# Kernel optimization log

Measured on AMD Instinct MI355X. Metric: run time of the kernel, lower is better.

## Reference

```python
import jax, jax.numpy as jnp
import numpy as np

# ---- system_parameters stand-ins (external module not in source) ----
D1, D2, D3 = 0.1, 1.0, 2.0
SIZE_X, SIZE_D = 5.0, 5.0
POWER_CONVERT = 10.0  # max power for opt_QoS stand-in
B, H, C = 8192, 96, 4
K1, K2 = 256, 256
D_IN = C + 2


def gamma_calculation(Hn):
    idx = np.arange(Hn)
    J = idx[:, None]  # row j
    I = idx[None, :]  # col i (time t)
    off = (D1 / 8.0 * (SIZE_X + SIZE_D) + D2 / 4.0) * (0.25 ** np.clip(I - 1 - J, 0, None))
    q = np.where(I == J, 2.0 * D1 * SIZE_X + D2, np.where(I > J, off, 0.0))
    gamma_list = q.sum(1)
    # Gamma_mat[j, t] = sum_{i>=t} q[j, i] for t >= j, else 0
    gmat = np.cumsum(q[:, ::-1], axis=1)[:, ::-1]
    gmat = np.where(I >= J, gmat, 0.0)
    return gamma_list.astype(np.float32), gmat.astype(np.float32), q.astype(np.float32)


def opt_qos(state, demand, power_max):
    # stand-in for external opt_QoS: action that serves demand and drains state
    # (nominal efficiency 0.8), capped at max power
    return jnp.minimum(jax.nn.relu(state + demand) / 0.8, power_max)


def setup_inputs() -> dict:
    key = jax.random.key(0)
    ks = jax.random.split(key, 9)
    kaiming = lambda k, shape: jax.random.normal(k, shape, jnp.float32) * np.sqrt(2.0 / shape[1])
    return {
        "policy_in_c": jax.random.uniform(ks[0], (B, H, C), jnp.float32) * 5.0,
        "trans_noise": jax.random.uniform(ks[1], (B, H, 1), jnp.float32) * 0.1,
        "demand_noise": jax.random.uniform(ks[2], (B, H, 1), jnp.float32) * 0.1,
        "action_pre": jax.random.uniform(ks[3], (B, 1), jnp.float32),
        "state_pre": jax.random.uniform(ks[4], (B, 1), jnp.float32) * 5.0,
        "Lambda": jnp.array([0.1], jnp.float32),
        "Budget": jnp.array([10.0], jnp.float32),
        "W1": kaiming(ks[5], (K1, D_IN)),
        "b1": jnp.zeros((K1,), jnp.float32),
        "W2": kaiming(ks[6], (K2, K1)),
        "b2": jnp.zeros((K2,), jnp.float32),
        "W3": kaiming(ks[7], (1, K2)),
        "b3": jnp.zeros((1,), jnp.float32),
    }


def reference(policy_in_c, trans_noise, demand_noise, action_pre, state_pre,
              Lambda, Budget, W1, b1, W2, b2, W3, b3):
    Bsz, Hn = policy_in_c.shape[0], policy_in_c.shape[1]
    gl_np, gmat_np, q_np = gamma_calculation(Hn)
    gamma_list = jnp.asarray(gl_np)                       # [H]
    q_cols = jnp.asarray(q_np.T)                          # q_cols[t] = q_mat[:, t]
    g_cols = jnp.asarray(np.concatenate([gmat_np[:, 1:].T,
                                         np.zeros((1, Hn), np.float32)], 0))  # g_cols[t] = Gamma_mat[:, t+1]
    per_step = Lambda * D3 + Budget / Hn                  # [1]
    bgt0 = per_step * jnp.ones((Bsz, 1), jnp.float32)

    def mlp(x):
        h1 = jax.nn.relu(x @ W1.T + b1)
        h2 = jax.nn.relu(h1 @ W2.T + b2)
        return jax.nn.relu(h2 @ W3.T + b3)

    def step(carry, xs):
        action_, state_, bgt, cum_c, dev, ad_prev = carry
        t, feat, noise, noise2, Gamma, q_col, g_col = xs
        a_ml = mlp(jnp.concatenate([feat, action_, state_], -1))
        demand = feat[:, :1]
        a_prior = opt_qos(state_, demand, POWER_CONVERT)
        sign = (a_ml < a_prior).astype(a_ml.dtype) * 2.0 - 1.0
        a_out = a_ml + jax.nn.relu(jnp.abs(a_ml - a_prior) - bgt / Gamma) * sign
        new_state = jnp.minimum(
            jax.nn.relu(state_ * (1.0 - noise2) + demand - (0.8 + noise) * a_out), 15.0)
        # ---- non-final-step branch (dev zero-padded to [B,H] so full matvec == sliced matmul) ----
        c_cost = D1 * new_state ** 2 + D2 * new_state + D3
        ad_new = jnp.abs(a_out - a_prior)
        dev_new = dev.at[:, t].set(ad_new[:, 0])
        cum_d = dev_new @ q_col                            # [B]
        c_prior = jnp.maximum(D3, c_cost - cum_d[:, None])
        cum_c_new = cum_c + (1.0 + Lambda) * c_prior - c_cost
        cum_d_g = dev_new @ g_col                          # [B]
        bgt_if = jnp.maximum(
            jax.nn.relu(bgt + per_step - ad_new * Gamma),
            cum_c_new - cum_d_g[:, None] + Lambda * D3 + (Budget / Hn) * (t + 2.0))
        # final step uses the stale action_diff from the previous iteration (as in source)
        bgt_else = jax.nn.relu(bgt + per_step - ad_prev * Gamma)
        is_last = t == Hn - 1
        bgt_next = jnp.where(is_last, bgt_else, bgt_if)
        cum_c_next = jnp.where(is_last, cum_c, cum_c_new)
        return (a_out, new_state, bgt_next, cum_c_next, dev_new, ad_new), a_out

    xs = (jnp.arange(Hn),
          jnp.transpose(policy_in_c, (1, 0, 2)),
          jnp.transpose(trans_noise, (1, 0, 2)),
          jnp.transpose(demand_noise, (1, 0, 2)),
          gamma_list, q_cols, g_cols)
    carry0 = (action_pre, state_pre, bgt0, jnp.zeros((Bsz, 1), jnp.float32),
              jnp.zeros((Bsz, Hn), jnp.float32), jnp.zeros((Bsz, 1), jnp.float32))
    _, ys = jax.lax.scan(step, carry0, xs)                 # ys: [H, B, 1]
    return jnp.transpose(ys[:, :, 0])                      # [B, H]
```

## Files before the change

### kernel.cpp

```cpp
#include <hip/hip_runtime.h>
#include <stdint.h>
#include <stddef.h>

typedef float    f32x4 __attribute__((ext_vector_type(4)));
typedef float    f32x2 __attribute__((ext_vector_type(2)));
typedef _Float16 f16x4 __attribute__((ext_vector_type(4)));
typedef _Float16 f16x8 __attribute__((ext_vector_type(8)));

#define HH 96
#define MROWS 16
#define OCT 136
#define NSTR 32
#define OSTR 100

#define DPP_ADD(v, ctrl) \
    ((v) + __builtin_bit_cast(float, __builtin_amdgcn_update_dpp( \
        0, __builtin_bit_cast(int, (v)), (ctrl), 0xF, 0xF, true)))

__launch_bounds__(256, 2)
__global__ void policy_scan_kernel(
    const float* __restrict__ policy,
    const float* __restrict__ noiseT,
    const float* __restrict__ noiseD,
    const float* __restrict__ action_pre,
    const float* __restrict__ state_pre,
    const float* __restrict__ Lambda1,
    const float* __restrict__ Budget1,
    const float* __restrict__ W1,
    const float* __restrict__ b1,
    const float* __restrict__ W2,
    const float* __restrict__ b2,
    const float* __restrict__ W3,
    const float* __restrict__ b3,
    float* __restrict__ out)
{
    __shared__ __attribute__((aligned(16))) float    featLDS[HH*MROWS*4];
    __shared__ __attribute__((aligned(16))) float    noiseTD[HH*NSTR];
    __shared__ __attribute__((aligned(16))) _Float16 h1LDS[32*OCT];
    __shared__ __attribute__((aligned(16))) float    partialLDS[MROWS*4];
    __shared__ __attribute__((aligned(16))) float    tblLDS[HH*4];
    __shared__ __attribute__((aligned(16))) float    outLDS[MROWS*OSTR];

    const int tid  = threadIdx.x;
    const int wave = tid >> 6;
    const int lane = tid & 63;
    const int l16  = lane & 15;
    const int lq   = lane >> 4;
    const int r0   = blockIdx.x * MROWS;

    {
        const f32x4* src = (const f32x4*)(policy + (size_t)r0 * HH * 4);
        #pragma unroll
        for (int i = 0; i < 6; ++i) {
            int idx = i*256 + tid;
            int row = idx / 96, t = idx - row*96;
            *(f32x4*)&featLDS[(t*MROWS + row)*4] = src[idx];
        }
        const float* s1 = noiseT + (size_t)r0 * HH;
        const float* s2 = noiseD + (size_t)r0 * HH;
        #pragma unroll
        for (int i = 0; i < 6; ++i) {
            int idx = i*256 + tid;
            int row = idx / 96, t = idx - row*96;
            noiseTD[t*NSTR + row*2    ] = s1[idx];
            noiseTD[t*NSTR + row*2 + 1] = s2[idx];
        }
    }
    const float lam  = Lambda1[0];
    const float budH = Budget1[0] * (1.0f/96.0f);
    const float b3s  = b3[0];
    const float per_step = lam * 2.0f + budH;
    if (tid < HH) {
        float e  = __builtin_exp2f(-2.0f * (float)(95 - tid));
        float ft = 0.5f * (1.0f - e);
        float G  = 2.0f + ft;
        *(f32x4*)&tblLDS[tid*4] = f32x4{ft, G, 1.0f/G, lam*2.0f + budH*((float)tid + 2.0f)};
    }

    f16x8 bfr[4][8];
    float b2v[4], w3v[4];
    #pragma unroll
    for (int tt = 0; tt < 4; ++tt) {
        const int n = wave*64 + tt*16 + l16;
        const float* wrow = W2 + (size_t)n * 256;
        #pragma unroll
        for (int kc = 0; kc < 8; ++kc) {
            const int k0 = kc*32 + lq*8;
            f32x4 u0 = *(const f32x4*)(wrow + k0);
            f32x4 u1 = *(const f32x4*)(wrow + k0 + 4);
            f16x8 v;
            v[0]=(_Float16)u0[0]; v[1]=(_Float16)u0[1]; v[2]=(_Float16)u0[2]; v[3]=(_Float16)u0[3];
            v[4]=(_Float16)u1[0]; v[5]=(_Float16)u1[1]; v[6]=(_Float16)u1[2]; v[7]=(_Float16)u1[3];
            bfr[tt][kc] = v;
        }
        b2v[tt] = b2[n];
        w3v[tt] = W3[n];
    }

    f16x8 w1A[4];
    #pragma unroll
    for (int tt = 0; tt < 4; ++tt) {
        f16x8 w = {};
        if (lq == 0) {
            const int nn = wave*64 + tt*16 + l16;
            #pragma unroll
            for (int j = 0; j < 6; ++j) w[j] = (_Float16)W1[nn*6 + j];
            w[6] = (_Float16)b1[nn];
        }
        w1A[tt] = w;
    }

    const int h1wbase = (wave*8 + (lq>>1))*OCT + l16*8 + (lq&1)*4;
    const int h1r     = lq*OCT + l16*8;

    float stA = action_pre[r0 + l16];
    float stS = state_pre[r0 + l16];
    float stB = per_step, stC = 0.0f, stSS = 0.0f, stAD = 0.0f;
    __syncthreads();

    #pragma unroll 1
    for (int t = 0; t < HH; ++t) {
        f32x4 f = *(const f32x4*)&featLDS[(t*MROWS + l16)*4];
        float dem = f[0];
        f16x8 xB = {};
        if (lq == 0) {
            xB[0]=(_Float16)f[0]; xB[1]=(_Float16)f[1];
            xB[2]=(_Float16)f[2]; xB[3]=(_Float16)f[3];
            xB[4]=(_Float16)stA;  xB[5]=(_Float16)stS;
            xB[6]=(_Float16)1.0f;
        }
        #pragma unroll
        for (int tt = 0; tt < 4; ++tt) {
            f32x4 g = {0.f,0.f,0.f,0.f};
            g = __builtin_amdgcn_mfma_f32_16x16x32_f16(w1A[tt], xB, g, 0, 0, 0);
            f16x4 hv;
            #pragma unroll
            for (int r = 0; r < 4; ++r) hv[r] = (_Float16)fmaxf(g[r], 0.0f);
            *(f16x4*)&h1LDS[h1wbase + tt*(2*OCT)] = hv;
        }
        __syncthreads();

        f32x4 acc[4];
        #pragma unroll
        for (int tt = 0; tt < 4; ++tt) acc[tt] = f32x4{0.f,0.f,0.f,0.f};
        #pragma unroll
        for (int kc = 0; kc < 8; ++kc) {
            f16x8 a = *(const f16x8*)&h1LDS[h1r + kc*(4*OCT)];
            #pragma unroll
            for (int tt = 0; tt < 4; ++tt)
                acc[tt] = __builtin_amdgcn_mfma_f32_16x16x32_f16(a, bfr[tt][kc], acc[tt], 0, 0, 0);
        }

        #pragma unroll
        for (int r = 0; r < 4; ++r) {
            float v = 0.f;
            #pragma unroll
            for (int tt = 0; tt < 4; ++tt)
                v = fmaf(w3v[tt], fmaxf(acc[tt][r] + b2v[tt], 0.0f), v);
            v = DPP_ADD(v, 0xB1);
            v = DPP_ADD(v, 0x4E);
            v = DPP_ADD(v, 0x124);
            v = DPP_ADD(v, 0x128);
            if (l16 == 0) partialLDS[(lq*4 + r)*4 + wave] = v;
        }
        __syncthreads();

        f32x4 q  = *(const f32x4*)&partialLDS[l16*4];
        f32x4 tb = *(const f32x4*)&tblLDS[t*4];
        f32x2 nz = *(const f32x2*)&noiseTD[t*NSTR + l16*2];
        float psum = (q[0] + q[1]) + (q[2] + q[3]);
        float a_ml   = fmaxf(psum + b3s, 0.0f);
        float a_prior = fminf(fmaxf(stS + dem, 0.0f) * 1.25f, 10.0f);
        float sgn    = (a_ml < a_prior) ? 1.0f : -1.0f;
        float a_out  = fmaf(fmaxf(fabsf(a_ml - a_prior) - stB * tb[2], 0.0f), sgn, a_ml);
        float ns     = fminf(fmaxf(stS * (1.0f - nz[1]) + dem - (0.8f + nz[0]) * a_out, 0.0f), 15.0f);
        float c_cost = fmaf(fmaf(0.1f, ns, 1.0f), ns, 2.0f);
        float ad_new = fabsf(a_out - a_prior);
        float cum_dv = fmaf(2.0f, ad_new, 0.375f * stSS);
        float c_prior = fmaxf(2.0f, c_cost - cum_dv);
        float cum_c_new = stC + (1.0f + lam) * c_prior - c_cost;
        float T      = fmaf(0.25f, stSS, ad_new);
        float cum_dg = tb[0] * T;
        float bgt_if = fmaxf(fmaxf(stB + per_step - ad_new * tb[1], 0.0f),
                             cum_c_new - cum_dg + tb[3]);
        float bgt_else = fmaxf(stB + per_step - stAD * tb[1], 0.0f);
        if (t == HH - 1) { stB = bgt_else; }
        else             { stB = bgt_if; stC = cum_c_new; }
        stSS = T;
        stAD = ad_new;
        stA  = a_out;
        stS  = ns;
        if (tid < MROWS) outLDS[tid*OSTR + t] = a_out;
    }

    __syncthreads();
    float* oslice = out + (size_t)r0 * HH;
    #pragma unroll
    for (int i = 0; i < 3; ++i) {
        int idx = (i*256 + tid) * 2;
        int row = idx / 96, c = idx - row*96;
        f32x2 v = { outLDS[row*OSTR + c], outLDS[row*OSTR + c + 1] };
        *(f32x2*)&oslice[idx] = v;
    }
}

extern "C" void kernel_launch(void* const* d_in, const int* in_sizes, int n_in,
                              void* d_out, int out_size, void* d_ws, size_t ws_size,
                              hipStream_t stream) {
    policy_scan_kernel<<<dim3(8192 / MROWS), dim3(256), 0, stream>>>(
        (const float*)d_in[0],
        (const float*)d_in[1],
        (const float*)d_in[2],
        (const float*)d_in[3],
        (const float*)d_in[4],
        (const float*)d_in[5],
        (const float*)d_in[6],
        (const float*)d_in[7],
        (const float*)d_in[8],
        (const float*)d_in[9],
        (const float*)d_in[10],
        (const float*)d_in[11],
        (const float*)d_in[12],
        (float*)d_out);
}
```

Measured before the change: 222.8 us.

## Compute layer-1 redundantly per wave in registers, dropping the h1 LDS round-trip and barrier

Each wave now computes every layer-1 activation itself with 16x16x16 MFMAs and feeds the packed f16 result straight into the layer-2 MFMA A operand. This removes the h1 shared-memory buffer and one __syncthreads per timestep from the serial scan loop. The partial-sum buffer is double-buffered so a single barrier per step is enough. The cost is 4x redundant layer-1 MFMA work and more registers for the W1 fragments, and W2's k-index mapping is reordered to match the new register layout.

```diff
diff --git a/kernel.cpp b/kernel.cpp
--- a/kernel.cpp
+++ b/kernel.cpp
@@ -4,18 +4,20 @@
 
 typedef float    f32x4 __attribute__((ext_vector_type(4)));
 typedef float    f32x2 __attribute__((ext_vector_type(2)));
+typedef _Float16 f16x2 __attribute__((ext_vector_type(2)));
 typedef _Float16 f16x4 __attribute__((ext_vector_type(4)));
 typedef _Float16 f16x8 __attribute__((ext_vector_type(8)));
 
 #define HH 96
 #define MROWS 16
-#define OCT 136
 #define NSTR 32
 #define OSTR 100
 
 #define DPP_ADD(v, ctrl) \
     ((v) + __builtin_bit_cast(float, __builtin_amdgcn_update_dpp( \
         0, __builtin_bit_cast(int, (v)), (ctrl), 0xF, 0xF, true)))
+
+#define CVT_PK(a, b) __builtin_bit_cast(f16x2, __builtin_amdgcn_cvt_pkrtz((a), (b)))
 
 __launch_bounds__(256, 2)
 __global__ void policy_scan_kernel(
@@ -34,12 +36,11 @@
     const float* __restrict__ b3,
     float* __restrict__ out)
 {
-    __shared__ __attribute__((aligned(16))) float    featLDS[HH*MROWS*4];
-    __shared__ __attribute__((aligned(16))) float    noiseTD[HH*NSTR];
-    __shared__ __attribute__((aligned(16))) _Float16 h1LDS[32*OCT];
-    __shared__ __attribute__((aligned(16))) float    partialLDS[MROWS*4];
-    __shared__ __attribute__((aligned(16))) float    tblLDS[HH*4];
-    __shared__ __attribute__((aligned(16))) float    outLDS[MROWS*OSTR];
+    __shared__ __attribute__((aligned(16))) float featLDS[HH*MROWS*4];
+    __shared__ __attribute__((aligned(16))) float noiseTD[HH*NSTR];
+    __shared__ __attribute__((aligned(16))) float partialLDS[2][MROWS*4];
+    __shared__ __attribute__((aligned(16))) float tblLDS[HH*4];
+    __shared__ __attribute__((aligned(16))) float outLDS[MROWS*OSTR];
 
     const int tid  = threadIdx.x;
     const int wave = tid >> 6;
@@ -85,9 +86,8 @@
         const float* wrow = W2 + (size_t)n * 256;
         #pragma unroll
         for (int kc = 0; kc < 8; ++kc) {
-            const int k0 = kc*32 + lq*8;
-            f32x4 u0 = *(const f32x4*)(wrow + k0);
-            f32x4 u1 = *(const f32x4*)(wrow + k0 + 4);
+            f32x4 u0 = *(const f32x4*)(wrow + kc*32 + lq*4);
+            f32x4 u1 = *(const f32x4*)(wrow + kc*32 + 16 + lq*4);
             f16x8 v;
             v[0]=(_Float16)u0[0]; v[1]=(_Float16)u0[1]; v[2]=(_Float16)u0[2]; v[3]=(_Float16)u0[3];
             v[4]=(_Float16)u1[0]; v[5]=(_Float16)u1[1]; v[6]=(_Float16)u1[2]; v[7]=(_Float16)u1[3];
@@ -97,21 +97,20 @@
         w3v[tt] = W3[n];
     }
 
-    f16x8 w1A[4];
+    f16x4 w1A[16];
     #pragma unroll
-    for (int tt = 0; tt < 4; ++tt) {
-        f16x8 w = {};
+    for (int q2 = 0; q2 < 16; ++q2) {
+        f16x4 w = {};
+        const int nn = q2*16 + l16;
         if (lq == 0) {
-            const int nn = wave*64 + tt*16 + l16;
-            #pragma unroll
-            for (int j = 0; j < 6; ++j) w[j] = (_Float16)W1[nn*6 + j];
-            w[6] = (_Float16)b1[nn];
-        }
-        w1A[tt] = w;
-    }
-
-    const int h1wbase = (wave*8 + (lq>>1))*OCT + l16*8 + (lq&1)*4;
-    const int h1r     = lq*OCT + l16*8;
+            w[0]=(_Float16)W1[nn*6+0]; w[1]=(_Float16)W1[nn*6+1];
+            w[2]=(_Float16)W1[nn*6+2]; w[3]=(_Float16)W1[nn*6+3];
+        } else if (lq == 1) {
+            w[0]=(_Float16)W1[nn*6+4]; w[1]=(_Float16)W1[nn*6+5];
+            w[2]=(_Float16)b1[nn];
+        }
+        w1A[q2] = w;
+    }
 
     float stA = action_pre[r0 + l16];
     float stS = state_pre[r0 + l16];
@@ -120,54 +119,55 @@
 
     #pragma unroll 1
     for (int t = 0; t < HH; ++t) {
-        f32x4 f = *(const f32x4*)&featLDS[(t*MROWS + l16)*4];
-        float dem = f[0];
-        f16x8 xB = {};
+        const f32x4 f  = *(const f32x4*)&featLDS[(t*MROWS + l16)*4];
+        const f32x4 tb = *(const f32x4*)&tblLDS[t*4];
+        const f32x2 nz = *(const f32x2*)&noiseTD[t*NSTR + l16*2];
+        const float dem = f[0];
+
+        f16x4 xB = {};
         if (lq == 0) {
             xB[0]=(_Float16)f[0]; xB[1]=(_Float16)f[1];
             xB[2]=(_Float16)f[2]; xB[3]=(_Float16)f[3];
-            xB[4]=(_Float16)stA;  xB[5]=(_Float16)stS;
-            xB[6]=(_Float16)1.0f;
-        }
-        #pragma unroll
-        for (int tt = 0; tt < 4; ++tt) {
-            f32x4 g = {0.f,0.f,0.f,0.f};
-            g = __builtin_amdgcn_mfma_f32_16x16x32_f16(w1A[tt], xB, g, 0, 0, 0);
-            f16x4 hv;
-            #pragma unroll
-            for (int r = 0; r < 4; ++r) hv[r] = (_Float16)fmaxf(g[r], 0.0f);
-            *(f16x4*)&h1LDS[h1wbase + tt*(2*OCT)] = hv;
-        }
-        __syncthreads();
+        } else if (lq == 1) {
+            xB[0]=(_Float16)stA; xB[1]=(_Float16)stS; xB[2]=(_Float16)1.0f;
+        }
 
         f32x4 acc[4];
         #pragma unroll
-        for (int tt = 0; tt < 4; ++tt) acc[tt] = f32x4{0.f,0.f,0.f,0.f};
+        for (int tt = 0; tt < 4; ++tt)
+            acc[tt] = f32x4{b2v[tt], b2v[tt], b2v[tt], b2v[tt]};
+
         #pragma unroll
         for (int kc = 0; kc < 8; ++kc) {
-            f16x8 a = *(const f16x8*)&h1LDS[h1r + kc*(4*OCT)];
+            const f32x4 z = {0.f, 0.f, 0.f, 0.f};
+            f32x4 g0 = __builtin_amdgcn_mfma_f32_16x16x16f16(w1A[2*kc    ], xB, z, 0, 0, 0);
+            f32x4 g1 = __builtin_amdgcn_mfma_f32_16x16x16f16(w1A[2*kc + 1], xB, z, 0, 0, 0);
+            f16x2 c0 = CVT_PK(g0[0], g0[1]);
+            f16x2 c1 = CVT_PK(g0[2], g0[3]);
+            f16x2 c2 = CVT_PK(g1[0], g1[1]);
+            f16x2 c3 = CVT_PK(g1[2], g1[3]);
+            f16x8 h = {c0[0],c0[1],c1[0],c1[1],c2[0],c2[1],c3[0],c3[1]};
+            const f16x8 hz = {};
+            h = __builtin_elementwise_max(h, hz);
             #pragma unroll
             for (int tt = 0; tt < 4; ++tt)
-                acc[tt] = __builtin_amdgcn_mfma_f32_16x16x32_f16(a, bfr[tt][kc], acc[tt], 0, 0, 0);
+                acc[tt] = __builtin_amdgcn_mfma_f32_16x16x32_f16(h, bfr[tt][kc], acc[tt], 0, 0, 0);
         }
 
         #pragma unroll
         for (int r = 0; r < 4; ++r) {
-            float v = 0.f;
-            #pragma unroll
-            for (int tt = 0; tt < 4; ++tt)
-                v = fmaf(w3v[tt], fmaxf(acc[tt][r] + b2v[tt], 0.0f), v);
+            float s0 = fmaf(w3v[0], fmaxf(acc[0][r], 0.0f), w3v[1] * fmaxf(acc[1][r], 0.0f));
+            float s1 = fmaf(w3v[2], fmaxf(acc[2][r], 0.0f), w3v[3] * fmaxf(acc[3][r], 0.0f));
+            float v = s0 + s1;
             v = DPP_ADD(v, 0xB1);
             v = DPP_ADD(v, 0x4E);
             v = DPP_ADD(v, 0x124);
             v = DPP_ADD(v, 0x128);
-            if (l16 == 0) partialLDS[(lq*4 + r)*4 + wave] = v;
+            if (l16 == 0) partialLDS[t & 1][(lq*4 + r)*4 + wave] = v;
         }
         __syncthreads();
 
-        f32x4 q  = *(const f32x4*)&partialLDS[l16*4];
-        f32x4 tb = *(const f32x4*)&tblLDS[t*4];
-        f32x2 nz = *(const f32x2*)&noiseTD[t*NSTR + l16*2];
+        const f32x4 q = *(const f32x4*)&partialLDS[t & 1][l16*4];
         float psum = (q[0] + q[1]) + (q[2] + q[3]);
         float a_ml   = fmaxf(psum + b3s, 0.0f);
         float a_prior = fminf(fmaxf(stS + dem, 0.0f) * 1.25f, 10.0f);
```

Result: slower. 243.1 us (+9.1%).

## Interleave two independent row groups per block to overlap scan latency

Applied to the files above, without the earlier changes.

Each block now handles two 16-row groups (P and Q) that are software-pipelined. One group's layer-2 MFMAs and scalar recurrence run while the other group's layer-1 and reduction are in flight, which hides the serial dependency chain of the time scan. The LDS staging of features, noise and outputs is removed. Inputs are prefetched one step ahead straight from global memory, and outputs are written directly to global. The b2 bias is folded into the accumulator initialisation. In exchange the block count halves and launch bounds drop to one block per SIMD, and output writes become strided and uncoalesced.

```diff
diff --git a/kernel.cpp b/kernel.cpp
--- a/kernel.cpp
+++ b/kernel.cpp
@@ -8,16 +8,41 @@
 typedef _Float16 f16x8 __attribute__((ext_vector_type(8)));
 
 #define HH 96
-#define MROWS 16
+#define RPB 32
 #define OCT 136
-#define NSTR 32
-#define OSTR 100
 
 #define DPP_ADD(v, ctrl) \
     ((v) + __builtin_bit_cast(float, __builtin_amdgcn_update_dpp( \
         0, __builtin_bit_cast(int, (v)), (ctrl), 0xF, 0xF, true)))
 
-__launch_bounds__(256, 2)
+struct SState { float A, S, B, C, SS, AD; };
+
+__device__ __forceinline__ float scan_update(
+    SState& st, float psum, float dem, f32x2 nz, f32x4 tb,
+    float b3s, float lam, float per_step, bool last)
+{
+    float a_ml   = fmaxf(psum + b3s, 0.0f);
+    float a_prior = fminf(fmaxf(st.S + dem, 0.0f) * 1.25f, 10.0f);
+    float sgn    = (a_ml < a_prior) ? 1.0f : -1.0f;
+    float a_out  = fmaf(fmaxf(fabsf(a_ml - a_prior) - st.B * tb[2], 0.0f), sgn, a_ml);
+    float ns     = fminf(fmaxf(st.S * (1.0f - nz[1]) + dem - (0.8f + nz[0]) * a_out, 0.0f), 15.0f);
+    float c_cost = fmaf(fmaf(0.1f, ns, 1.0f), ns, 2.0f);
+    float ad_new = fabsf(a_out - a_prior);
+    float cum_dv = fmaf(2.0f, ad_new, 0.375f * st.SS);
+    float c_prior = fmaxf(2.0f, c_cost - cum_dv);
+    float cum_c_new = st.C + (1.0f + lam) * c_prior - c_cost;
+    float T      = fmaf(0.25f, st.SS, ad_new);
+    float cum_dg = tb[0] * T;
+    float bgt_if = fmaxf(fmaxf(st.B + per_step - ad_new * tb[1], 0.0f),
+                         cum_c_new - cum_dg + tb[3]);
+    float bgt_else = fmaxf(st.B + per_step - st.AD * tb[1], 0.0f);
+    if (last) { st.B = bgt_else; }
+    else      { st.B = bgt_if; st.C = cum_c_new; }
+    st.SS = T; st.AD = ad_new; st.A = a_out; st.S = ns;
+    return a_out;
+}
+
+__launch_bounds__(256, 1)
 __global__ void policy_scan_kernel(
     const float* __restrict__ policy,
     const float* __restrict__ noiseT,
@@ -34,38 +59,19 @@
     const float* __restrict__ b3,
     float* __restrict__ out)
 {
-    __shared__ __attribute__((aligned(16))) float    featLDS[HH*MROWS*4];
-    __shared__ __attribute__((aligned(16))) float    noiseTD[HH*NSTR];
-    __shared__ __attribute__((aligned(16))) _Float16 h1LDS[32*OCT];
-    __shared__ __attribute__((aligned(16))) float    partialLDS[MROWS*4];
+    __shared__ __attribute__((aligned(16))) _Float16 h1P[32*OCT];
+    __shared__ __attribute__((aligned(16))) _Float16 h1Q[32*OCT];
+    __shared__ __attribute__((aligned(16))) float    partP[16*4];
+    __shared__ __attribute__((aligned(16))) float    partQ[16*4];
     __shared__ __attribute__((aligned(16))) float    tblLDS[HH*4];
-    __shared__ __attribute__((aligned(16))) float    outLDS[MROWS*OSTR];
 
     const int tid  = threadIdx.x;
     const int wave = tid >> 6;
     const int lane = tid & 63;
     const int l16  = lane & 15;
     const int lq   = lane >> 4;
-    const int r0   = blockIdx.x * MROWS;
-
-    {
-        const f32x4* src = (const f32x4*)(policy + (size_t)r0 * HH * 4);
-        #pragma unroll
-        for (int i = 0; i < 6; ++i) {
-            int idx = i*256 + tid;
-            int row = idx / 96, t = idx - row*96;
-            *(f32x4*)&featLDS[(t*MROWS + row)*4] = src[idx];
-        }
-        const float* s1 = noiseT + (size_t)r0 * HH;
-        const float* s2 = noiseD + (size_t)r0 * HH;
-        #pragma unroll
-        for (int i = 0; i < 6; ++i) {
-            int idx = i*256 + tid;
-            int row = idx / 96, t = idx - row*96;
-            noiseTD[t*NSTR + row*2    ] = s1[idx];
-            noiseTD[t*NSTR + row*2 + 1] = s2[idx];
-        }
-    }
+    const int r0   = blockIdx.x * RPB;
+
     const float lam  = Lambda1[0];
     const float budH = Budget1[0] * (1.0f/96.0f);
     const float b3s  = b3[0];
@@ -113,101 +119,166 @@
     const int h1wbase = (wave*8 + (lq>>1))*OCT + l16*8 + (lq&1)*4;
     const int h1r     = lq*OCT + l16*8;
 
-    float stA = action_pre[r0 + l16];
-    float stS = state_pre[r0 + l16];
-    float stB = per_step, stC = 0.0f, stSS = 0.0f, stAD = 0.0f;
+    const float* pP  = policy + (size_t)(r0 + l16)      * (HH*4);
+    const float* pQ  = policy + (size_t)(r0 + 16 + l16) * (HH*4);
+    const float* tPp = noiseT + (size_t)(r0 + l16)      * HH;
+    const float* tQp = noiseT + (size_t)(r0 + 16 + l16) * HH;
+    const float* dPp = noiseD + (size_t)(r0 + l16)      * HH;
+    const float* dQp = noiseD + (size_t)(r0 + 16 + l16) * HH;
+
+    SState stP = { action_pre[r0 + l16],      state_pre[r0 + l16],      per_step, 0.f, 0.f, 0.f };
+    SState stQ = { action_pre[r0 + 16 + l16], state_pre[r0 + 16 + l16], per_step, 0.f, 0.f, 0.f };
+
+    f32x4 fP  = *(const f32x4*)(pP);
+    f32x4 fQ  = *(const f32x4*)(pQ);
+    f32x2 nzP = { tPp[0], dPp[0] };
+    f32x2 nzQ = { tQp[0], dQp[0] };
+
+    f32x4 accP[4], accQ[4];
+    #pragma unroll
+    for (int tt = 0; tt < 4; ++tt) accQ[tt] = f32x4{0.f,0.f,0.f,0.f};
+
+    float demQprev = 0.f;
+    f32x2 nzQprev  = {0.f, 0.f};
+    f32x4 tbQprev  = {0.f, 0.f, 0.f, 0.f};
+
     __syncthreads();
 
     #pragma unroll 1
     for (int t = 0; t < HH; ++t) {
-        f32x4 f = *(const f32x4*)&featLDS[(t*MROWS + l16)*4];
-        float dem = f[0];
-        f16x8 xB = {};
-        if (lq == 0) {
-            xB[0]=(_Float16)f[0]; xB[1]=(_Float16)f[1];
-            xB[2]=(_Float16)f[2]; xB[3]=(_Float16)f[3];
-            xB[4]=(_Float16)stA;  xB[5]=(_Float16)stS;
-            xB[6]=(_Float16)1.0f;
-        }
-        #pragma unroll
-        for (int tt = 0; tt < 4; ++tt) {
-            f32x4 g = {0.f,0.f,0.f,0.f};
-            g = __builtin_amdgcn_mfma_f32_16x16x32_f16(w1A[tt], xB, g, 0, 0, 0);
-            f16x4 hv;
-            #pragma unroll
-            for (int r = 0; r < 4; ++r) hv[r] = (_Float16)fmaxf(g[r], 0.0f);
-            *(f16x4*)&h1LDS[h1wbase + tt*(2*OCT)] = hv;
+        const f32x4 tbP = *(const f32x4*)&tblLDS[t*4];
+
+        {
+            f16x8 xB = {};
+            if (lq == 0) {
+                xB[0]=(_Float16)fP[0]; xB[1]=(_Float16)fP[1];
+                xB[2]=(_Float16)fP[2]; xB[3]=(_Float16)fP[3];
+                xB[4]=(_Float16)stP.A; xB[5]=(_Float16)stP.S;
+                xB[6]=(_Float16)1.0f;
+            }
+            #pragma unroll
+            for (int tt = 0; tt < 4; ++tt) {
+                f32x4 g = {0.f,0.f,0.f,0.f};
+                g = __builtin_amdgcn_mfma_f32_16x16x32_f16(w1A[tt], xB, g, 0, 0, 0);
+                f16x4 hv;
+                #pragma unroll
+                for (int r = 0; r < 4; ++r) hv[r] = (_Float16)fmaxf(g[r], 0.0f);
+                *(f16x4*)&h1P[h1wbase + tt*(2*OCT)] = hv;
+            }
+        }
+
+        if (t > 0) {
+            #pragma unroll
+            for (int r = 0; r < 4; ++r) {
+                float s0 = fmaf(w3v[0], fmaxf(accQ[0][r], 0.0f), w3v[1] * fmaxf(accQ[1][r], 0.0f));
+                float s1 = fmaf(w3v[2], fmaxf(accQ[2][r], 0.0f), w3v[3] * fmaxf(accQ[3][r], 0.0f));
+                float v = s0 + s1;
+                v = DPP_ADD(v, 0xB1); v = DPP_ADD(v, 0x4E);
+                v = DPP_ADD(v, 0x124); v = DPP_ADD(v, 0x128);
+                if (l16 == 0) partQ[(lq*4 + r)*4 + wave] = v;
+            }
         }
         __syncthreads();
 
-        f32x4 acc[4];
-        #pragma unroll
-        for (int tt = 0; tt < 4; ++tt) acc[tt] = f32x4{0.f,0.f,0.f,0.f};
+        #pragma unroll
+        for (int tt = 0; tt < 4; ++tt) accP[tt] = f32x4{b2v[tt], b2v[tt], b2v[tt], b2v[tt]};
         #pragma unroll
         for (int kc = 0; kc < 8; ++kc) {
-            f16x8 a = *(const f16x8*)&h1LDS[h1r + kc*(4*OCT)];
+            f16x8 a = *(const f16x8*)&h1P[h1r + kc*(4*OCT)];
             #pragma unroll
             for (int tt = 0; tt < 4; ++tt)
-                acc[tt] = __builtin_amdgcn_mfma_f32_16x16x32_f16(a, bfr[tt][kc], acc[tt], 0, 0, 0);
+                accP[tt] = __builtin_amdgcn_mfma_f32_16x16x32_f16(a, bfr[tt][kc], accP[tt], 0, 0, 0);
+        }
+
+        const int tn = (t < HH-1) ? t+1 : HH-1;
+        f32x4 fPn  = *(const f32x4*)(pP + tn*4);
+        f32x4 fQn  = *(const f32x4*)(pQ + tn*4);
+        f32x2 nzPn = { tPp[tn], dPp[tn] };
+        f32x2 nzQn = { tQp[tn], dQp[tn] };
+
+        if (t > 0) {
+            f32x4 qq = *(const f32x4*)&partQ[l16*4];
+            float psum = (qq[0] + qq[1]) + (qq[2] + qq[3]);
+            float aQ = scan_update(stQ, psum, demQprev, nzQprev, tbQprev,
+                                   b3s, lam, per_step, false);
+            if (tid < 16) out[(size_t)(r0 + 16 + tid)*HH + (t-1)] = aQ;
+        }
+
+        {
+            f16x8 xB = {};
+            if (lq == 0) {
+                xB[0]=(_Float16)fQ[0]; xB[1]=(_Float16)fQ[1];
+                xB[2]=(_Float16)fQ[2]; xB[3]=(_Float16)fQ[3];
+                xB[4]=(_Float16)stQ.A; xB[5]=(_Float16)stQ.S;
+                xB[6]=(_Float16)1.0f;
+            }
+            #pragma unroll
+            for (int tt = 0; tt < 4; ++tt) {
+                f32x4 g = {0.f,0.f,0.f,0.f};
+                g = __builtin_amdgcn_mfma_f32_16x16x32_f16(w1A[tt], xB, g, 0, 0, 0);
+                f16x4 hv;
+                #pragma unroll
+                for (int r = 0; r < 4; ++r) hv[r] = (_Float16)fmaxf(g[r], 0.0f);
+                *(f16x4*)&h1Q[h1wbase + tt*(2*OCT)] = hv;
+            }
+            demQprev = fQ[0]; nzQprev = nzQ; tbQprev = tbP;
         }
 
         #pragma unroll
         for (int r = 0; r < 4; ++r) {
-            float v = 0.f;
+            float s0 = fmaf(w3v[0], fmaxf(accP[0][r], 0.0f), w3v[1] * fmaxf(accP[1][r], 0.0f));
+            float s1 = fmaf(w3v[2], fmaxf(accP[2][r], 0.0f), w3v[3] * fmaxf(accP[3][r], 0.0f));
+            float v = s0 + s1;
+            v = DPP_ADD(v, 0xB1); v = DPP_ADD(v, 0x4E);
+            v = DPP_ADD(v, 0x124); v = DPP_ADD(v, 0x128);
+            if (l16 == 0) partP[(lq*4 + r)*4 + wave] = v;
+        }
+        __syncthreads();
+
+        #pragma unroll
+        for (int tt = 0; tt < 4; ++tt) accQ[tt] = f32x4{b2v[tt], b2v[tt], b2v[tt], b2v[tt]};
+        #pragma unroll
+        for (int kc = 0; kc < 8; ++kc) {
+            f16x8 a = *(const f16x8*)&h1Q[h1r + kc*(4*OCT)];
             #pragma unroll
             for (int tt = 0; tt < 4; ++tt)
-                v = fmaf(w3v[tt], fmaxf(acc[tt][r] + b2v[tt], 0.0f), v);
-            v = DPP_ADD(v, 0xB1);
-            v = DPP_ADD(v, 0x4E);
-            v = DPP_ADD(v, 0x124);
-            v = DPP_ADD(v, 0x128);
-            if (l16 == 0) partialLDS[(lq*4 + r)*4 + wave] = v;
-        }
-        __syncthreads();
-
-        f32x4 q  = *(const f32x4*)&partialLDS[l16*4];
-        f32x4 tb = *(const f32x4*)&tblLDS[t*4];
-        f32x2 nz = *(const f32x2*)&noiseTD[t*NSTR + l16*2];
-        float psum = (q[0] + q[1]) + (q[2] + q[3]);
-        float a_ml   = fmaxf(psum + b3s, 0.0f);
-        float a_prior = fminf(fmaxf(stS + dem, 0.0f) * 1.25f, 10.0f);
-        float sgn    = (a_ml < a_prior) ? 1.0f : -1.0f;
-        float a_out  = fmaf(fmaxf(fabsf(a_ml - a_prior) - stB * tb[2], 0.0f), sgn, a_ml);
-        float ns     = fminf(fmaxf(stS * (1.0f - nz[1]) + dem - (0.8f + nz[0]) * a_out, 0.0f), 15.0f);
-        float c_cost = fmaf(fmaf(0.1f, ns, 1.0f), ns, 2.0f);
-        float ad_new = fabsf(a_out - a_prior);
-        float cum_dv = fmaf(2.0f, ad_new, 0.375f * stSS);
-        float c_prior = fmaxf(2.0f, c_cost - cum_dv);
-        float cum_c_new = stC + (1.0f + lam) * c_prior - c_cost;
-        float T      = fmaf(0.25f, stSS, ad_new);
-        float cum_dg = tb[0] * T;
-        float bgt_if = fmaxf(fmaxf(stB + per_step - ad_new * tb[1], 0.0f),
-                             cum_c_new - cum_dg + tb[3]);
-        float bgt_else = fmaxf(stB + per_step - stAD * tb[1], 0.0f);
-        if (t == HH - 1) { stB = bgt_else; }
-        else             { stB = bgt_if; stC = cum_c_new; }
-        stSS = T;
-        stAD = ad_new;
-        stA  = a_out;
-        stS  = ns;
-        if (tid < MROWS) outLDS[tid*OSTR + t] = a_out;
-    }
-
+                accQ[tt] = __builtin_amdgcn_mfma_f32_16x16x32_f16(a, bfr[tt][kc], accQ[tt], 0, 0, 0);
+        }
+
+        {
+            f32x4 qp = *(const f32x4*)&partP[l16*4];
+            float psum = (qp[0] + qp[1]) + (qp[2] + qp[3]);
+            float aP = scan_update(stP, psum, fP[0], nzP, tbP,
+                                   b3s, lam, per_step, t == HH-1);
+            if (tid < 16) out[(size_t)(r0 + tid)*HH + t] = aP;
+        }
+
+        fP = fPn; fQ = fQn; nzP = nzPn; nzQ = nzQn;
+    }
+
+    #pragma unroll
+    for (int r = 0; r < 4; ++r) {
+        float s0 = fmaf(w3v[0], fmaxf(accQ[0][r], 0.0f), w3v[1] * fmaxf(accQ[1][r], 0.0f));
+        float s1 = fmaf(w3v[2], fmaxf(accQ[2][r], 0.0f), w3v[3] * fmaxf(accQ[3][r], 0.0f));
+        float v = s0 + s1;
+        v = DPP_ADD(v, 0xB1); v = DPP_ADD(v, 0x4E);
+        v = DPP_ADD(v, 0x124); v = DPP_ADD(v, 0x128);
+        if (l16 == 0) partQ[(lq*4 + r)*4 + wave] = v;
+    }
     __syncthreads();
-    float* oslice = out + (size_t)r0 * HH;
-    #pragma unroll
-    for (int i = 0; i < 3; ++i) {
-        int idx = (i*256 + tid) * 2;
-        int row = idx / 96, c = idx - row*96;
-        f32x2 v = { outLDS[row*OSTR + c], outLDS[row*OSTR + c + 1] };
-        *(f32x2*)&oslice[idx] = v;
+    {
+        f32x4 qq = *(const f32x4*)&partQ[l16*4];
+        float psum = (qq[0] + qq[1]) + (qq[2] + qq[3]);
+        float aQ = scan_update(stQ, psum, demQprev, nzQprev, tbQprev,
+                               b3s, lam, per_step, true);
+        if (tid < 16) out[(size_t)(r0 + 16 + tid)*HH + (HH-1)] = aQ;
     }
 }
 
 extern "C" void kernel_launch(void* const* d_in, const int* in_sizes, int n_in,
                               void* d_out, int out_size, void* d_ws, size_t ws_size,
                               hipStream_t stream) {
-    policy_scan_kernel<<<dim3(8192 / MROWS), dim3(256), 0, stream>>>(
+    policy_scan_kernel<<<dim3(8192 / RPB), dim3(256), 0, stream>>>(
         (const float*)d_in[0],
         (const float*)d_in[1],
         (const float*)d_in[2],
```

Result: slower. 279.0 us (+25.2%).

## Split hidden-layer columns across eight waves per block instead of four

Applied to the files above, without the earlier changes.

Doubles the block to 512 threads so each wave handles 32 of the 256 hidden units instead of 64. This halves the per-wave MFMA chain and register footprint in the sequential per-timestep loop, with occupancy raised via launch bounds. It also folds the b2 bias into the accumulator initialisation. In exchange the two per-step block barriers now synchronise eight waves, and the partial-sum reduction reads twice as many values.

```diff
diff --git a/kernel.cpp b/kernel.cpp
--- a/kernel.cpp
+++ b/kernel.cpp
@@ -17,7 +17,7 @@
     ((v) + __builtin_bit_cast(float, __builtin_amdgcn_update_dpp( \
         0, __builtin_bit_cast(int, (v)), (ctrl), 0xF, 0xF, true)))
 
-__launch_bounds__(256, 2)
+__launch_bounds__(512, 4)
 __global__ void policy_scan_kernel(
     const float* __restrict__ policy,
     const float* __restrict__ noiseT,
@@ -37,12 +37,12 @@
     __shared__ __attribute__((aligned(16))) float    featLDS[HH*MROWS*4];
     __shared__ __attribute__((aligned(16))) float    noiseTD[HH*NSTR];
     __shared__ __attribute__((aligned(16))) _Float16 h1LDS[32*OCT];
-    __shared__ __attribute__((aligned(16))) float    partialLDS[MROWS*4];
+    __shared__ __attribute__((aligned(16))) float    partialLDS[MROWS*8];
     __shared__ __attribute__((aligned(16))) float    tblLDS[HH*4];
     __shared__ __attribute__((aligned(16))) float    outLDS[MROWS*OSTR];
 
     const int tid  = threadIdx.x;
-    const int wave = tid >> 6;
+    const int wv   = tid >> 6;
     const int lane = tid & 63;
     const int l16  = lane & 15;
     const int lq   = lane >> 4;
@@ -51,16 +51,16 @@
     {
         const f32x4* src = (const f32x4*)(policy + (size_t)r0 * HH * 4);
         #pragma unroll
-        for (int i = 0; i < 6; ++i) {
-            int idx = i*256 + tid;
+        for (int i = 0; i < 3; ++i) {
+            int idx = i*512 + tid;
             int row = idx / 96, t = idx - row*96;
             *(f32x4*)&featLDS[(t*MROWS + row)*4] = src[idx];
         }
         const float* s1 = noiseT + (size_t)r0 * HH;
         const float* s2 = noiseD + (size_t)r0 * HH;
         #pragma unroll
-        for (int i = 0; i < 6; ++i) {
-            int idx = i*256 + tid;
+        for (int i = 0; i < 3; ++i) {
+            int idx = i*512 + tid;
             int row = idx / 96, t = idx - row*96;
             noiseTD[t*NSTR + row*2    ] = s1[idx];
             noiseTD[t*NSTR + row*2 + 1] = s2[idx];
@@ -77,11 +77,11 @@
         *(f32x4*)&tblLDS[tid*4] = f32x4{ft, G, 1.0f/G, lam*2.0f + budH*((float)tid + 2.0f)};
     }
 
-    f16x8 bfr[4][8];
-    float b2v[4], w3v[4];
+    f16x8 bfr[2][8];
+    float b2v[2], w3v[2];
     #pragma unroll
-    for (int tt = 0; tt < 4; ++tt) {
-        const int n = wave*64 + tt*16 + l16;
+    for (int tt = 0; tt < 2; ++tt) {
+        const int n = wv*32 + tt*16 + l16;
         const float* wrow = W2 + (size_t)n * 256;
         #pragma unroll
         for (int kc = 0; kc < 8; ++kc) {
@@ -97,12 +97,12 @@
         w3v[tt] = W3[n];
     }
 
-    f16x8 w1A[4];
+    f16x8 w1A[2];
     #pragma unroll
-    for (int tt = 0; tt < 4; ++tt) {
+    for (int tt = 0; tt < 2; ++tt) {
         f16x8 w = {};
         if (lq == 0) {
-            const int nn = wave*64 + tt*16 + l16;
+            const int nn = wv*32 + tt*16 + l16;
             #pragma unroll
             for (int j = 0; j < 6; ++j) w[j] = (_Float16)W1[nn*6 + j];
             w[6] = (_Float16)b1[nn];
@@ -110,7 +110,7 @@
         w1A[tt] = w;
     }
 
-    const int h1wbase = (wave*8 + (lq>>1))*OCT + l16*8 + (lq&1)*4;
+    const int h1wbase = (wv*4 + (lq>>1))*OCT + l16*8 + (lq&1)*4;
     const int h1r     = lq*OCT + l16*8;
 
     float stA = action_pre[r0 + l16];
@@ -130,7 +130,7 @@
             xB[6]=(_Float16)1.0f;
         }
         #pragma unroll
-        for (int tt = 0; tt < 4; ++tt) {
+        for (int tt = 0; tt < 2; ++tt) {
             f32x4 g = {0.f,0.f,0.f,0.f};
             g = __builtin_amdgcn_mfma_f32_16x16x32_f16(w1A[tt], xB, g, 0, 0, 0);
             f16x4 hv;
@@ -140,35 +140,32 @@
         }
         __syncthreads();
 
-        f32x4 acc[4];
-        #pragma unroll
-        for (int tt = 0; tt < 4; ++tt) acc[tt] = f32x4{0.f,0.f,0.f,0.f};
+        f32x4 acc0 = f32x4{b2v[0], b2v[0], b2v[0], b2v[0]};
+        f32x4 acc1 = f32x4{b2v[1], b2v[1], b2v[1], b2v[1]};
         #pragma unroll
         for (int kc = 0; kc < 8; ++kc) {
             f16x8 a = *(const f16x8*)&h1LDS[h1r + kc*(4*OCT)];
-            #pragma unroll
-            for (int tt = 0; tt < 4; ++tt)
-                acc[tt] = __builtin_amdgcn_mfma_f32_16x16x32_f16(a, bfr[tt][kc], acc[tt], 0, 0, 0);
+            acc0 = __builtin_amdgcn_mfma_f32_16x16x32_f16(a, bfr[0][kc], acc0, 0, 0, 0);
+            acc1 = __builtin_amdgcn_mfma_f32_16x16x32_f16(a, bfr[1][kc], acc1, 0, 0, 0);
         }
 
         #pragma unroll
         for (int r = 0; r < 4; ++r) {
-            float v = 0.f;
-            #pragma unroll
-            for (int tt = 0; tt < 4; ++tt)
-                v = fmaf(w3v[tt], fmaxf(acc[tt][r] + b2v[tt], 0.0f), v);
+            float v = fmaf(w3v[0], fmaxf(acc0[r], 0.0f), w3v[1] * fmaxf(acc1[r], 0.0f));
             v = DPP_ADD(v, 0xB1);
             v = DPP_ADD(v, 0x4E);
             v = DPP_ADD(v, 0x124);
             v = DPP_ADD(v, 0x128);
-            if (l16 == 0) partialLDS[(lq*4 + r)*4 + wave] = v;
+            if (l16 == 0) partialLDS[(lq*4 + r)*8 + wv] = v;
         }
         __syncthreads();
 
-        f32x4 q  = *(const f32x4*)&partialLDS[l16*4];
+        f32x4 q0 = *(const f32x4*)&partialLDS[l16*8];
+        f32x4 q1 = *(const f32x4*)&partialLDS[l16*8 + 4];
         f32x4 tb = *(const f32x4*)&tblLDS[t*4];
         f32x2 nz = *(const f32x2*)&noiseTD[t*NSTR + l16*2];
-        float psum = (q[0] + q[1]) + (q[2] + q[3]);
+        float psum = ((q0[0] + q0[1]) + (q0[2] + q0[3]))
+                   + ((q1[0] + q1[1]) + (q1[2] + q1[3]));
         float a_ml   = fmaxf(psum + b3s, 0.0f);
         float a_prior = fminf(fmaxf(stS + dem, 0.0f) * 1.25f, 10.0f);
         float sgn    = (a_ml < a_prior) ? 1.0f : -1.0f;
@@ -197,17 +194,16 @@
     float* oslice = out + (size_t)r0 * HH;
     #pragma unroll
     for (int i = 0; i < 3; ++i) {
-        int idx = (i*256 + tid) * 2;
+        int idx = i*512 + tid;
         int row = idx / 96, c = idx - row*96;
-        f32x2 v = { outLDS[row*OSTR + c], outLDS[row*OSTR + c + 1] };
-        *(f32x2*)&oslice[idx] = v;
+        oslice[idx] = outLDS[row*OSTR + c];
     }
 }
 
 extern "C" void kernel_launch(void* const* d_in, const int* in_sizes, int n_in,
                               void* d_out, int out_size, void* d_ws, size_t ws_size,
                               hipStream_t stream) {
-    policy_scan_kernel<<<dim3(8192 / MROWS), dim3(256), 0, stream>>>(
+    policy_scan_kernel<<<dim3(8192 / MROWS), dim3(512), 0, stream>>>(
         (const float*)d_in[0],
         (const float*)d_in[1],
         (const float*)d_in[2],
```

After: 243.2 us. +9.1%, slower.
